# Kernel tuning notes

Hardware: AMD Instinct MI355X
Metric: run time of the kernel (lower is better)

Reference implementation:

```python
import jax, jax.numpy as jnp
import numpy as np

M = 16384      # total flat points per role (8 scenes x 2048 pts)
D = 256        # d_model
H = 4          # heads
K = 16         # knn neighbors
DFF = 1024     # 4*D
LN_EPS = 1e-5


def _ln(x, g, b):
    m = jnp.mean(x, axis=-1, keepdims=True)
    v = jnp.mean((x - m) ** 2, axis=-1, keepdims=True)
    return (x - m) / jnp.sqrt(v + LN_EPS) * g + b


def _knn_block(x, coord, ctx, ctx_coord, idx,
               Wq, Wk, Wv, Wo, g1, b1, pe_w, pe_b,
               W1, bf1, W2, bf2, g2, b2):
    # x: [M,D] query feats; ctx: [N,D] context feats; idx: [M,K] neighbor ids (-1 = invalid)
    m, d = x.shape
    k = idx.shape[1]
    dh = d // H
    valid = idx >= 0
    idx_c = jnp.where(valid, idx, 0)

    xn = _ln(x, g1, b1)
    q = (xn @ Wq).reshape(m, H, dh)                      # [M,H,dh]
    k_all = ctx @ Wk                                     # [N,D]
    v_all = ctx @ Wv                                     # [N,D]

    rel = coord[:, None, :] - ctx_coord[idx_c]           # [M,K,3]
    pe = rel @ pe_w + pe_b                               # [M,K,D] relative position encoding
    kg = (k_all[idx_c] + pe).reshape(m, k, H, dh)        # gathered keys  [M,K,H,dh]
    vg = (v_all[idx_c] + pe).reshape(m, k, H, dh)        # gathered values

    scale = jnp.asarray(1.0 / np.sqrt(dh), x.dtype)
    scores = jnp.einsum('mhd,mkhd->mhk', q, kg) * scale
    scores = jnp.where(valid[:, None, :], scores, jnp.asarray(-1e9, x.dtype))
    attn = jax.nn.softmax(scores, axis=-1)
    out = jnp.einsum('mhk,mkhd->mhd', attn, vg).reshape(m, d) @ Wo
    x = x + out
    h = jax.nn.gelu(_ln(x, g2, b2) @ W1 + bf1)
    return x + (h @ W2 + bf2)


def setup_inputs() -> dict:
    key = jax.random.key(0)
    ks = jax.random.split(key, 24)
    s = 0.02
    nblk = 2  # [0]=self(a), [1]=cross(a,b)
    inp = {
        'feat_a': jax.random.normal(ks[0], (M, D), jnp.float32),
        'coord_a': jax.random.normal(ks[1], (M, 3), jnp.float32),
        'feat_b': jax.random.normal(ks[2], (M, D), jnp.float32),
        'coord_b': jax.random.normal(ks[3], (M, 3), jnp.float32),
        'Wq': jax.random.normal(ks[4], (nblk, D, D), jnp.float32) * s,
        'Wk': jax.random.normal(ks[5], (nblk, D, D), jnp.float32) * s,
        'Wv': jax.random.normal(ks[6], (nblk, D, D), jnp.float32) * s,
        'Wo': jax.random.normal(ks[7], (nblk, D, D), jnp.float32) * s,
        'ln1_g': jnp.ones((nblk, D), jnp.float32),
        'ln1_b': jnp.zeros((nblk, D), jnp.float32),
        'pe_w': jax.random.normal(ks[8], (nblk, 3, D), jnp.float32) * s,
        'pe_b': jnp.zeros((nblk, D), jnp.float32),
        'ffn_w1': jax.random.normal(ks[9], (nblk, D, DFF), jnp.float32) * s,
        'ffn_b1': jnp.zeros((nblk, DFF), jnp.float32),
        'ffn_w2': jax.random.normal(ks[10], (nblk, DFF, D), jnp.float32) * s,
        'ffn_b2': jnp.zeros((nblk, D), jnp.float32),
        'ln2_g': jnp.ones((nblk, D), jnp.float32),
        'ln2_b': jnp.zeros((nblk, D), jnp.float32),
        'knn_a2a': jax.random.randint(ks[11], (M, K), 0, M, jnp.int64 if jax.config.jax_enable_x64 else jnp.int32),
        'knn_a2b': jax.random.randint(ks[12], (M, K), 0, M, jnp.int64 if jax.config.jax_enable_x64 else jnp.int32),
    }
    return inp


def reference(feat_a, coord_a, feat_b, coord_b,
              Wq, Wk, Wv, Wo, ln1_g, ln1_b, pe_w, pe_b,
              ffn_w1, ffn_b1, ffn_w2, ffn_b2, ln2_g, ln2_b,
              knn_a2a, knn_a2b):
    def params(i):
        return (Wq[i], Wk[i], Wv[i], Wo[i], ln1_g[i], ln1_b[i], pe_w[i], pe_b[i],
                ffn_w1[i], ffn_b1[i], ffn_w2[i], ffn_b2[i], ln2_g[i], ln2_b[i])
    # layer 'self(a)': feat[a] = block(feat[a], coord[a], knn_indexes['a2a'])
    fa = _knn_block(feat_a, coord_a, feat_a, coord_a, knn_a2a, *params(0))
    # layer 'cross(a,b)': feat[a] = block(query=feat[a], context=feat[b], knn_indexes['a2b'])
    fa = _knn_block(fa, coord_a, feat_b, coord_b, knn_a2b, *params(1))
    return fa
```

## Files before the change

### kernel.cpp

```cpp
#include <hip/hip_runtime.h>
#include <hip/hip_bf16.h>
#include <stdint.h>

#define MM 16384
#define DD 256
#define HH 4
#define KK 16
#define DFF_ 1024

typedef __attribute__((ext_vector_type(8))) short bf16x8;
typedef __attribute__((ext_vector_type(16))) float f32x16;

__device__ __forceinline__ unsigned short f2bf(float f) {
    unsigned u = __builtin_bit_cast(unsigned, f);
    unsigned r = u + 0x7fffu + ((u >> 16) & 1u);
    return (unsigned short)(r >> 16);
}
__device__ __forceinline__ float bf2f(unsigned short h) {
    unsigned u = ((unsigned)h) << 16;
    return __builtin_bit_cast(float, u);
}
__device__ __forceinline__ float bflo(unsigned u) { return __builtin_bit_cast(float, u << 16); }
__device__ __forceinline__ float bfhi(unsigned u) { return __builtin_bit_cast(float, u & 0xffff0000u); }


__global__ __launch_bounds__(256) void prep_weights(
        const float* __restrict__ Wq, const float* __restrict__ Wk,
        const float* __restrict__ Wv, const float* __restrict__ Wo,
        const float* __restrict__ W1, const float* __restrict__ W2,
        unsigned short* __restrict__ wf) {
    int t = blockIdx.x * blockDim.x + threadIdx.x;
    const float* src; unsigned short* dst;
    int kd, nsrc, rem, blk, e, sect;
    if (t < 131072) { sect = 0; rem = t; blk = rem >> 16; e = rem & 65535;
        src = Wq; dst = wf + blk * 65536; kd = 256; nsrc = 256; }
    else if (t < 262144) { sect = 1; rem = t - 131072; blk = rem >> 16; e = rem & 65535;
        src = Wk; dst = wf + 131072 + blk * 131072; kd = 256; nsrc = 256; }
    else if (t < 393216) { sect = 2; rem = t - 262144; blk = rem >> 16; e = rem & 65535;
        src = Wv; dst = wf + 131072 + blk * 131072; kd = 256; nsrc = 256; }
    else if (t < 524288) { sect = 0; rem = t - 393216; blk = rem >> 16; e = rem & 65535;
        src = Wo; dst = wf + 393216 + blk * 65536; kd = 256; nsrc = 256; }
    else if (t < 1048576) { sect = 0; rem = t - 524288; blk = rem >> 18; e = rem & 262143;
        src = W1; dst = wf + 524288 + blk * 262144; kd = 256; nsrc = 1024; }
    else if (t < 1572864) { sect = 0; rem = t - 1048576; blk = rem >> 18; e = rem & 262143;
        src = W2; dst = wf + 1048576 + blk * 262144; kd = 1024; nsrc = 256; }
    else return;
    int k = e / nsrc;
    int n = e - k * nsrc;
    if (sect == 1) n = (n >> 2) * 8 + (n & 3);
    else if (sect == 2) n = (n >> 2) * 8 + 4 + (n & 3);
    float v = src[(size_t)blk * kd * nsrc + e];
    int off = ((n >> 5) * (kd >> 4) + (k >> 4)) * 512 + (((k >> 3) & 1) * 32 + (n & 31)) * 8 + (k & 7);
    dst[off] = f2bf(v);
}

__global__ __launch_bounds__(256) void ln_to_frag(
        const float* __restrict__ x, const float* __restrict__ g,
        const float* __restrict__ b, unsigned short* __restrict__ out,
        int apply_ln) {
    int wave = threadIdx.x >> 6, lane = threadIdx.x & 63;
    int m = blockIdx.x * 4 + wave;
    const float4 xv = reinterpret_cast<const float4*>(x + (size_t)m * DD)[lane];
    float vals[4] = {xv.x, xv.y, xv.z, xv.w};
    int k0 = lane * 4;
    if (apply_ln) {
        float s = vals[0] + vals[1] + vals[2] + vals[3];
        float sq = vals[0]*vals[0] + vals[1]*vals[1] + vals[2]*vals[2] + vals[3]*vals[3];
        for (int o = 32; o; o >>= 1) { s += __shfl_xor(s, o, 64); sq += __shfl_xor(sq, o, 64); }
        float mean = s * (1.0f / DD);
        float var = sq * (1.0f / DD) - mean * mean;
        float rs = rsqrtf(var + 1e-5f);
        #pragma unroll
        for (int c = 0; c < 4; ++c)
            vals[c] = (vals[c] - mean) * rs * g[k0 + c] + b[k0 + c];
    }
    int chunk = ((m >> 5) * (DD >> 4) + (k0 >> 4)) * 64 + ((k0 >> 3) & 1) * 32 + (m & 31);
    ushort4 o4 = make_ushort4(f2bf(vals[0]), f2bf(vals[1]), f2bf(vals[2]), f2bf(vals[3]));
    *reinterpret_cast<ushort4*>(out + (size_t)chunk * 8 + (k0 & 7)) = o4;
}

constexpr int GOUT_F32 = 0;
constexpr int GOUT_BF16 = 1;
constexpr int GOUT_GELU_FRAG = 2;

template <int KGH>
__device__ __forceinline__ void compute_tile(
        const bf16x8* __restrict__ a0, const bf16x8* __restrict__ a1,
        const bf16x8* __restrict__ b0, const bf16x8* __restrict__ b1,
        f32x16 acc[2][2]) {
    #pragma unroll 4
    for (int g = 0; g < KGH; ++g) {
        bf16x8 av0 = a0[g * 64];
        bf16x8 av1 = a1[g * 64];
        bf16x8 bv0 = b0[g * 64];
        bf16x8 bv1 = b1[g * 64];
        acc[0][0] = __builtin_amdgcn_mfma_f32_32x32x16_bf16(av0, bv0, acc[0][0], 0, 0, 0);
        acc[0][1] = __builtin_amdgcn_mfma_f32_32x32x16_bf16(av0, bv1, acc[0][1], 0, 0, 0);
        acc[1][0] = __builtin_amdgcn_mfma_f32_32x32x16_bf16(av1, bv0, acc[1][0], 0, 0, 0);
        acc[1][1] = __builtin_amdgcn_mfma_f32_32x32x16_bf16(av1, bv1, acc[1][1], 0, 0, 0);
    }
}

template <int KD, int NOUT, int SPLITK, int MODE, bool RESID, bool BIAS>
__global__ __launch_bounds__(SPLITK * 128) void gemm_frag(
        const bf16x8* __restrict__ A, const bf16x8* __restrict__ B,
        void* __restrict__ outp, const float* __restrict__ resid,
        const float* __restrict__ bias, int out_kd) {
    static_assert(MODE != GOUT_GELU_FRAG || SPLITK == 1, "gelu path is 2-wave only");
    constexpr int KG = KD / 16;
    constexpr int KGH = KG / SPLITK;
    __shared__ float lds[SPLITK == 2 ? 2 * 64 * 64 : 2 * 32 * 33];
    int wave = threadIdx.x >> 6, lane = threadIdx.x & 63;
    int mhalf = wave & 1;
    int khalf = (SPLITK == 2) ? (wave >> 1) : 0;
    int m0 = blockIdx.x * 128 + mhalf * 64;
    int n0 = blockIdx.y * 64;
    const bf16x8* a0 = A + ((size_t)(m0 >> 5) * KG + khalf * KGH) * 64 + lane;
    const bf16x8* a1 = a0 + (size_t)KG * 64;
    const bf16x8* b0 = B + ((size_t)(n0 >> 5) * KG + khalf * KGH) * 64 + lane;
    const bf16x8* b1 = b0 + (size_t)KG * 64;
    f32x16 acc[2][2] = {};
    compute_tile<KGH>(a0, a1, b0, b1, acc);
    int col = lane & 31, rq = (lane >> 5) * 4;
    if constexpr (SPLITK == 2) {
        if (khalf == 1) {
            #pragma unroll
            for (int i = 0; i < 2; ++i)
            #pragma unroll
            for (int j = 0; j < 2; ++j)
            #pragma unroll
            for (int r = 0; r < 16; ++r) {
                int row = (r & 3) + 8 * (r >> 2) + rq + i * 32;
                lds[mhalf * 4096 + row * 64 + j * 32 + col] = acc[i][j][r];
            }
        }
        __syncthreads();
        if (khalf == 1) return;
        #pragma unroll
        for (int i = 0; i < 2; ++i)
        #pragma unroll
        for (int j = 0; j < 2; ++j)
        #pragma unroll
        for (int r = 0; r < 16; ++r) {
            int row = (r & 3) + 8 * (r >> 2) + rq + i * 32;
            acc[i][j][r] += lds[mhalf * 4096 + row * 64 + j * 32 + col];
        }
    }
    if constexpr (MODE != GOUT_GELU_FRAG) {
        #pragma unroll
        for (int i = 0; i < 2; ++i)
        #pragma unroll
        for (int j = 0; j < 2; ++j) {
            #pragma unroll
            for (int r = 0; r < 16; ++r) {
                int row = (r & 3) + 8 * (r >> 2) + rq;
                int m = m0 + i * 32 + row;
                int n = n0 + j * 32 + col;
                float v = acc[i][j][r];
                if (BIAS) v += bias[n];
                if (RESID) v += resid[(size_t)m * NOUT + n];
                if (MODE == GOUT_F32) ((float*)outp)[(size_t)m * NOUT + n] = v;
                else ((unsigned short*)outp)[(size_t)m * NOUT + n] = f2bf(v);
            }
        }
    } else {
        float* wlds = &lds[wave * 1056];
        for (int i = 0; i < 2; ++i)
        for (int j = 0; j < 2; ++j) {
            #pragma unroll
            for (int r = 0; r < 16; ++r) {
                int row = (r & 3) + 8 * (r >> 2) + rq;
                int n = n0 + j * 32 + col;
                float v = acc[i][j][r] + bias[n];
                float arg = v * (1.5957691216f + 0.0713548163f * v * v);
                v = v * __frcp_rn(1.0f + __expf(-arg));
                wlds[row * 33 + col] = v;
            }
            #pragma unroll
            for (int it = 0; it < 2; ++it) {
                int task = lane + it * 64;
                int row = task >> 2, cc = task & 3;
                int m = m0 + i * 32 + row;
                int k = n0 + j * 32 + cc * 8;
                float* p = &wlds[row * 33 + cc * 8];
                unsigned short us[8];
                #pragma unroll
                for (int e = 0; e < 8; ++e) us[e] = f2bf(p[e]);
                int chunk = ((m >> 5) * (out_kd >> 4) + (k >> 4)) * 64 + ((k >> 3) & 1) * 32 + (m & 31);
                reinterpret_cast<uint4*>(outp)[chunk] = *reinterpret_cast<uint4*>(us);
            }
        }
    }
}

__global__ __launch_bounds__(256) void gemm_qkv(
        const bf16x8* __restrict__ Aq, const bf16x8* __restrict__ Akv,
        const bf16x8* __restrict__ Bq, const bf16x8* __restrict__ Bkv,
        unsigned short* __restrict__ qout, unsigned short* __restrict__ kvout) {
    constexpr int KG = 16, KGH = 8;
    __shared__ float lds[2 * 64 * 64];
    int wave = threadIdx.x >> 6, lane = threadIdx.x & 63;
    int mhalf = wave & 1, khalf = wave >> 1;
    int y = blockIdx.y;
    bool isQ = y < 4;
    const bf16x8* A = isQ ? Aq : Akv;
    const bf16x8* B = isQ ? Bq : Bkv;
    unsigned short* out = isQ ? qout : kvout;
    int nstride = isQ ? 256 : 512;
    int n0 = (isQ ? y : y - 4) * 64;
    int m0 = blockIdx.x * 128 + mhalf * 64;
    const bf16x8* a0 = A + ((size_t)(m0 >> 5) * KG + khalf * KGH) * 64 + lane;
    const bf16x8* a1 = a0 + (size_t)KG * 64;
    const bf16x8* b0 = B + ((size_t)(n0 >> 5) * KG + khalf * KGH) * 64 + lane;
    const bf16x8* b1 = b0 + (size_t)KG * 64;
    f32x16 acc[2][2] = {};
    compute_tile<KGH>(a0, a1, b0, b1, acc);
    int col = lane & 31, rq = (lane >> 5) * 4;
    if (khalf == 1) {
        #pragma unroll
        for (int i = 0; i < 2; ++i)
        #pragma unroll
        for (int j = 0; j < 2; ++j)
        #pragma unroll
        for (int r = 0; r < 16; ++r) {
            int row = (r & 3) + 8 * (r >> 2) + rq + i * 32;
            lds[mhalf * 4096 + row * 64 + j * 32 + col] = acc[i][j][r];
        }
    }
    __syncthreads();
    if (khalf == 1) return;
    #pragma unroll
    for (int i = 0; i < 2; ++i)
    #pragma unroll
    for (int j = 0; j < 2; ++j)
    #pragma unroll
    for (int r = 0; r < 16; ++r) {
        int row = (r & 3) + 8 * (r >> 2) + rq;
        float v = acc[i][j][r] + lds[mhalf * 4096 + (row + i * 32) * 64 + j * 32 + col];
        out[(size_t)(m0 + i * 32 + row) * nstride + n0 + j * 32 + col] = f2bf(v);
    }
}

__global__ __launch_bounds__(256) void attn_kernel(
        const unsigned short* __restrict__ q, const unsigned short* __restrict__ kv,
        const float* __restrict__ coord, const float* __restrict__ ctx_coord,
        const int* __restrict__ knn,
        const float* __restrict__ pe_w, const float* __restrict__ pe_b,
        unsigned short* __restrict__ out_frag) {
    int wave = threadIdx.x >> 6, lane = threadIdx.x & 63;
    int m = blockIdx.x * 4 + wave;
    int s = lane & 15;
    int d0 = (lane >> 4) * 64 + s * 4;

    ushort4 qv4 = *reinterpret_cast<const ushort4*>(q + (size_t)m * DD + d0);
    float qx = bf2f(qv4.x), qy = bf2f(qv4.y), qz = bf2f(qv4.z), qw = bf2f(qv4.w);
    float4 pw0 = *reinterpret_cast<const float4*>(pe_w + d0);
    float4 pw1 = *reinterpret_cast<const float4*>(pe_w + DD + d0);
    float4 pw2 = *reinterpret_cast<const float4*>(pe_w + 2 * DD + d0);
    float4 pbv = *reinterpret_cast<const float4*>(pe_b + d0);

    float cx = coord[m * 3], cy = coord[m * 3 + 1], cz = coord[m * 3 + 2];
    int myidx = knn[(size_t)m * KK + s];
    int icm = myidx < 0 ? 0 : myidx;
    float rx = cx - ctx_coord[icm * 3];
    float ry = cy - ctx_coord[icm * 3 + 1];
    float rz = cz - ctx_coord[icm * 3 + 2];

    float t0 = qx * pw0.x + qy * pw0.y + qz * pw0.z + qw * pw0.w;
    float t1 = qx * pw1.x + qy * pw1.y + qz * pw1.z + qw * pw1.w;
    float t2 = qx * pw2.x + qy * pw2.y + qz * pw2.z + qw * pw2.w;
    float t3 = qx * pbv.x + qy * pbv.y + qz * pbv.z + qw * pbv.w;
    #pragma unroll
    for (int o = 1; o < 16; o <<= 1) {
        t0 += __shfl_xor(t0, o, 64);
        t1 += __shfl_xor(t1, o, 64);
        t2 += __shfl_xor(t2, o, 64);
        t3 += __shfl_xor(t3, o, 64);
    }

    float sc_own = 0.0f;
    unsigned vlo[KK], vhi[KK];
    #pragma unroll
    for (int j = 0; j < KK; ++j) {
        int ij = __shfl(myidx, j, 64);
        int ic = ij < 0 ? 0 : ij;
        uint4 kvv = *reinterpret_cast<const uint4*>(kv + (size_t)ic * 512 + (size_t)(d0 >> 2) * 8);
        vlo[j] = kvv.z; vhi[j] = kvv.w;
        float p = qx * bflo(kvv.x) + qy * bfhi(kvv.x)
                + qz * bflo(kvv.y) + qw * bfhi(kvv.y);
        p += __shfl_xor(p, 1, 64);
        p += __shfl_xor(p, 2, 64);
        p += __shfl_xor(p, 4, 64);
        p += __shfl_xor(p, 8, 64);
        sc_own = (j == s) ? p : sc_own;
    }
    float corr = rx * t0 + ry * t1 + rz * t2 + t3;
    sc_own = (myidx >= 0) ? (sc_own + corr) * 0.125f : -1e9f;

    float mx = sc_own;
    mx = fmaxf(mx, __shfl_xor(mx, 1, 64));
    mx = fmaxf(mx, __shfl_xor(mx, 2, 64));
    mx = fmaxf(mx, __shfl_xor(mx, 4, 64));
    mx = fmaxf(mx, __shfl_xor(mx, 8, 64));
    float e = __expf(sc_own - mx);
    float sum = e;
    sum += __shfl_xor(sum, 1, 64);
    sum += __shfl_xor(sum, 2, 64);
    sum += __shfl_xor(sum, 4, 64);
    sum += __shfl_xor(sum, 8, 64);
    float w_own = e * __frcp_rn(sum);

    float wrx = w_own * rx, wry = w_own * ry, wrz = w_own * rz;
    #pragma unroll
    for (int o = 1; o < 16; o <<= 1) {
        wrx += __shfl_xor(wrx, o, 64);
        wry += __shfl_xor(wry, o, 64);
        wrz += __shfl_xor(wrz, o, 64);
    }

    int gbase = lane & 48;
    float ax = 0.f, ay = 0.f, az = 0.f, aw = 0.f;
    #pragma unroll
    for (int j = 0; j < KK; ++j) {
        float wj = __shfl(w_own, gbase + j, 64);
        ax += wj * bflo(vlo[j]);
        ay += wj * bfhi(vlo[j]);
        az += wj * bflo(vhi[j]);
        aw += wj * bfhi(vhi[j]);
    }
    ax += wrx * pw0.x + wry * pw1.x + wrz * pw2.x + pbv.x;
    ay += wrx * pw0.y + wry * pw1.y + wrz * pw2.y + pbv.y;
    az += wrx * pw0.z + wry * pw1.z + wrz * pw2.z + pbv.z;
    aw += wrx * pw0.w + wry * pw1.w + wrz * pw2.w + pbv.w;

    ushort4 o4 = make_ushort4(f2bf(ax), f2bf(ay), f2bf(az), f2bf(aw));
    int chunk = ((m >> 5) * (DD >> 4) + (d0 >> 4)) * 64 + ((d0 >> 3) & 1) * 32 + (m & 31);
    *reinterpret_cast<ushort4*>(out_frag + (size_t)chunk * 8 + (d0 & 7)) = o4;
}

extern "C" void kernel_launch(void* const* d_in, const int* in_sizes, int n_in,
                              void* d_out, int out_size, void* d_ws, size_t ws_size,
                              hipStream_t stream) {
    const float* feat_a = (const float*)d_in[0];
    const float* coord_a = (const float*)d_in[1];
    const float* feat_b = (const float*)d_in[2];
    const float* coord_b = (const float*)d_in[3];
    const float* Wq = (const float*)d_in[4];
    const float* Wk = (const float*)d_in[5];
    const float* Wv = (const float*)d_in[6];
    const float* Wo = (const float*)d_in[7];
    const float* ln1_g = (const float*)d_in[8];
    const float* ln1_b = (const float*)d_in[9];
    const float* pe_w = (const float*)d_in[10];
    const float* pe_b = (const float*)d_in[11];
    const float* W1 = (const float*)d_in[12];
    const float* b1 = (const float*)d_in[13];
    const float* W2 = (const float*)d_in[14];
    const float* b2 = (const float*)d_in[15];
    const float* ln2_g = (const float*)d_in[16];
    const float* ln2_b = (const float*)d_in[17];
    const int* knn_a2a = (const int*)d_in[18];
    const int* knn_a2b = (const int*)d_in[19];

    char* ws = (char*)d_ws;
    unsigned short* wfrag = (unsigned short*)ws;
    float* xmid = (float*)(ws + (4ull << 20));
    float* xout0 = (float*)(ws + (20ull << 20));
    unsigned short* qbuf = (unsigned short*)(ws + (36ull << 20));
    unsigned short* kvbuf = (unsigned short*)(ws + (52ull << 20));
    unsigned short* xnf = (unsigned short*)(ws + (68ull << 20));
    unsigned short* ctxf = (unsigned short*)(ws + (76ull << 20));
    unsigned short* attnf = (unsigned short*)(ws + (84ull << 20));
    unsigned short* geluf = (unsigned short*)(ws + (36ull << 20));

    const unsigned short* WQF = wfrag;
    const unsigned short* KVF = wfrag + 131072;
    const unsigned short* WOF = wfrag + 393216;
    const unsigned short* W1F = wfrag + 524288;
    const unsigned short* W2F = wfrag + 1048576;

    prep_weights<<<(1572864 + 255) / 256, 256, 0, stream>>>(Wq, Wk, Wv, Wo, W1, W2, wfrag);

    for (int blk = 0; blk < 2; ++blk) {
        const float* x_in = blk ? xout0 : feat_a;
        const float* ctx = blk ? feat_b : feat_a;
        const float* ccrd = blk ? coord_b : coord_a;
        const int* knn = blk ? knn_a2b : knn_a2a;
        float* x_out_final = blk ? (float*)d_out : xout0;

        ln_to_frag<<<MM / 4, 256, 0, stream>>>(ctx, nullptr, nullptr, ctxf, 0);
        ln_to_frag<<<MM / 4, 256, 0, stream>>>(x_in, ln1_g + blk * DD, ln1_b + blk * DD, xnf, 1);

        gemm_qkv<<<dim3(MM / 128, 12), 256, 0, stream>>>(
            (const bf16x8*)xnf, (const bf16x8*)ctxf,
            (const bf16x8*)(WQF + blk * 65536), (const bf16x8*)(KVF + blk * 131072),
            qbuf, kvbuf);

        attn_kernel<<<MM / 4, 256, 0, stream>>>(qbuf, kvbuf, coord_a, ccrd, knn,
                                                pe_w + blk * 3 * DD, pe_b + blk * DD, attnf);

        gemm_frag<256, 256, 2, GOUT_F32, true, false><<<dim3(MM / 128, 4), 256, 0, stream>>>(
            (const bf16x8*)attnf, (const bf16x8*)(WOF + blk * 65536), xmid, x_in, nullptr, 0);

        ln_to_frag<<<MM / 4, 256, 0, stream>>>(xmid, ln2_g + blk * DD, ln2_b + blk * DD, xnf, 1);

        gemm_frag<256, 1024, 1, GOUT_GELU_FRAG, false, true><<<dim3(MM / 128, 16), 128, 0, stream>>>(
            (const bf16x8*)xnf, (const bf16x8*)(W1F + blk * 262144), geluf, nullptr,
            b1 + blk * DFF_, 1024);

        gemm_frag<1024, 256, 2, GOUT_F32, true, true><<<dim3(MM / 128, 4), 256, 0, stream>>>(
            (const bf16x8*)geluf, (const bf16x8*)(W2F + blk * 262144), x_out_final, xmid,
            b2 + blk * DD, 0);
    }
}
```

Before: 365.9 us.

## Fuse LayerNorm into residual GEMM epilogues with full-row tiles

Replaces the output-projection and FFN2 GEMMs with a 512-thread kernel where each block computes a full 64x256 row tile. Row statistics are reduced across waves through shared memory, so the next LayerNorm (ln2, or the next block's ln1) is applied in the epilogue and written directly in fragment layout. This removes separate ln_to_frag launches and their re-read of the fp32 activations. In exchange it uses more shared memory, adds extra barriers, and launches fewer, larger blocks, which may lower occupancy.

```diff
diff --git a/kernel.cpp b/kernel.cpp
--- a/kernel.cpp
+++ b/kernel.cpp
@@ -79,10 +79,6 @@
     *reinterpret_cast<ushort4*>(out + (size_t)chunk * 8 + (k0 & 7)) = o4;
 }
 
-constexpr int GOUT_F32 = 0;
-constexpr int GOUT_BF16 = 1;
-constexpr int GOUT_GELU_FRAG = 2;
-
 template <int KGH>
 __device__ __forceinline__ void compute_tile(
         const bf16x8* __restrict__ a0, const bf16x8* __restrict__ a1,
@@ -101,80 +97,100 @@
     }
 }
 
-template <int KD, int NOUT, int SPLITK, int MODE, bool RESID, bool BIAS>
-__global__ __launch_bounds__(SPLITK * 128) void gemm_frag(
+template <int KD, bool BIAS, bool DO_LN>
+__global__ __launch_bounds__(512) void gemm_ln(
         const bf16x8* __restrict__ A, const bf16x8* __restrict__ B,
-        void* __restrict__ outp, const float* __restrict__ resid,
-        const float* __restrict__ bias, int out_kd) {
-    static_assert(MODE != GOUT_GELU_FRAG || SPLITK == 1, "gelu path is 2-wave only");
-    constexpr int KG = KD / 16;
-    constexpr int KGH = KG / SPLITK;
-    __shared__ float lds[SPLITK == 2 ? 2 * 64 * 64 : 2 * 32 * 33];
+        const float* __restrict__ resid, const float* __restrict__ bias,
+        const float* __restrict__ lng, const float* __restrict__ lnb,
+        float* __restrict__ out_f32, unsigned short* __restrict__ out_frag) {
+    constexpr int KG = KD / 16, KGH = KG / 2;
+    __shared__ float lds[4 * 64 * 64 + 512 + 128];
+    float* lnsum = lds + 16384;
+    float* lnsq  = lnsum + 256;
+    float* lnstat = lnsq + 256;
     int wave = threadIdx.x >> 6, lane = threadIdx.x & 63;
-    int mhalf = wave & 1;
-    int khalf = (SPLITK == 2) ? (wave >> 1) : 0;
-    int m0 = blockIdx.x * 128 + mhalf * 64;
-    int n0 = blockIdx.y * 64;
-    const bf16x8* a0 = A + ((size_t)(m0 >> 5) * KG + khalf * KGH) * 64 + lane;
+    int wn = wave & 3, kh = wave >> 2;
+    int m0 = blockIdx.x * 64;
+    int n0 = wn * 64;
+    const bf16x8* a0 = A + ((size_t)(m0 >> 5) * KG + kh * KGH) * 64 + lane;
     const bf16x8* a1 = a0 + (size_t)KG * 64;
-    const bf16x8* b0 = B + ((size_t)(n0 >> 5) * KG + khalf * KGH) * 64 + lane;
+    const bf16x8* b0 = B + ((size_t)(n0 >> 5) * KG + kh * KGH) * 64 + lane;
     const bf16x8* b1 = b0 + (size_t)KG * 64;
     f32x16 acc[2][2] = {};
     compute_tile<KGH>(a0, a1, b0, b1, acc);
     int col = lane & 31, rq = (lane >> 5) * 4;
-    if constexpr (SPLITK == 2) {
-        if (khalf == 1) {
+    float* skbuf = &lds[wn * 4096];
+    if (kh == 1) {
+        #pragma unroll
+        for (int i = 0; i < 2; ++i)
+        #pragma unroll
+        for (int j = 0; j < 2; ++j)
+        #pragma unroll
+        for (int r = 0; r < 16; ++r) {
+            int rl = (r & 3) + 8 * (r >> 2) + rq;
+            skbuf[(i * 32 + rl) * 64 + j * 32 + col] = acc[i][j][r];
+        }
+    }
+    __syncthreads();
+    if (kh == 0) {
+        #pragma unroll
+        for (int i = 0; i < 2; ++i)
+        #pragma unroll
+        for (int j = 0; j < 2; ++j)
+        #pragma unroll
+        for (int r = 0; r < 16; ++r) {
+            int rl = (r & 3) + 8 * (r >> 2) + rq;
+            int m = m0 + i * 32 + rl;
+            int n = n0 + j * 32 + col;
+            float v = acc[i][j][r] + skbuf[(i * 32 + rl) * 64 + j * 32 + col];
+            if (BIAS) v += bias[n];
+            v += resid[(size_t)m * 256 + n];
+            out_f32[(size_t)m * 256 + n] = v;
+            acc[i][j][r] = v;
+        }
+    }
+    if constexpr (DO_LN) {
+        if (kh == 0) {
             #pragma unroll
             for (int i = 0; i < 2; ++i)
             #pragma unroll
-            for (int j = 0; j < 2; ++j)
-            #pragma unroll
             for (int r = 0; r < 16; ++r) {
-                int row = (r & 3) + 8 * (r >> 2) + rq + i * 32;
-                lds[mhalf * 4096 + row * 64 + j * 32 + col] = acc[i][j][r];
+                float v0 = acc[i][0][r], v1 = acc[i][1][r];
+                float p = v0 + v1, q = v0 * v0 + v1 * v1;
+                #pragma unroll
+                for (int o = 1; o < 32; o <<= 1) {
+                    p += __shfl_xor(p, o, 64);
+                    q += __shfl_xor(q, o, 64);
+                }
+                if (col == 0) {
+                    int row64 = i * 32 + (r & 3) + 8 * (r >> 2) + rq;
+                    lnsum[wn * 64 + row64] = p;
+                    lnsq[wn * 64 + row64] = q;
+                }
             }
         }
         __syncthreads();
-        if (khalf == 1) return;
-        #pragma unroll
-        for (int i = 0; i < 2; ++i)
-        #pragma unroll
-        for (int j = 0; j < 2; ++j)
-        #pragma unroll
-        for (int r = 0; r < 16; ++r) {
-            int row = (r & 3) + 8 * (r >> 2) + rq + i * 32;
-            acc[i][j][r] += lds[mhalf * 4096 + row * 64 + j * 32 + col];
-        }
-    }
-    if constexpr (MODE != GOUT_GELU_FRAG) {
-        #pragma unroll
-        for (int i = 0; i < 2; ++i)
-        #pragma unroll
-        for (int j = 0; j < 2; ++j) {
-            #pragma unroll
-            for (int r = 0; r < 16; ++r) {
-                int row = (r & 3) + 8 * (r >> 2) + rq;
-                int m = m0 + i * 32 + row;
-                int n = n0 + j * 32 + col;
-                float v = acc[i][j][r];
-                if (BIAS) v += bias[n];
-                if (RESID) v += resid[(size_t)m * NOUT + n];
-                if (MODE == GOUT_F32) ((float*)outp)[(size_t)m * NOUT + n] = v;
-                else ((unsigned short*)outp)[(size_t)m * NOUT + n] = f2bf(v);
-            }
-        }
-    } else {
-        float* wlds = &lds[wave * 1056];
+        if (wave == 0) {
+            int row = lane;
+            float s = lnsum[row] + lnsum[64 + row] + lnsum[128 + row] + lnsum[192 + row];
+            float q = lnsq[row] + lnsq[64 + row] + lnsq[128 + row] + lnsq[192 + row];
+            float mean = s * (1.0f / 256.0f);
+            float var = q * (1.0f / 256.0f) - mean * mean;
+            lnstat[row * 2] = mean;
+            lnstat[row * 2 + 1] = rsqrtf(var + 1e-5f);
+        }
+        __syncthreads();
+        if (kh == 1) return;
         for (int i = 0; i < 2; ++i)
         for (int j = 0; j < 2; ++j) {
             #pragma unroll
             for (int r = 0; r < 16; ++r) {
-                int row = (r & 3) + 8 * (r >> 2) + rq;
+                int rl = (r & 3) + 8 * (r >> 2) + rq;
+                int row64 = i * 32 + rl;
+                float mean = lnstat[row64 * 2], rs = lnstat[row64 * 2 + 1];
                 int n = n0 + j * 32 + col;
-                float v = acc[i][j][r] + bias[n];
-                float arg = v * (1.5957691216f + 0.0713548163f * v * v);
-                v = v * __frcp_rn(1.0f + __expf(-arg));
-                wlds[row * 33 + col] = v;
+                float vln = (acc[i][j][r] - mean) * rs * lng[n] + lnb[n];
+                skbuf[rl * 33 + col] = vln;
             }
             #pragma unroll
             for (int it = 0; it < 2; ++it) {
@@ -182,13 +198,56 @@
                 int row = task >> 2, cc = task & 3;
                 int m = m0 + i * 32 + row;
                 int k = n0 + j * 32 + cc * 8;
-                float* p = &wlds[row * 33 + cc * 8];
+                float* p = &skbuf[row * 33 + cc * 8];
                 unsigned short us[8];
                 #pragma unroll
                 for (int e = 0; e < 8; ++e) us[e] = f2bf(p[e]);
-                int chunk = ((m >> 5) * (out_kd >> 4) + (k >> 4)) * 64 + ((k >> 3) & 1) * 32 + (m & 31);
-                reinterpret_cast<uint4*>(outp)[chunk] = *reinterpret_cast<uint4*>(us);
+                int chunk = ((m >> 5) * 16 + (k >> 4)) * 64 + ((k >> 3) & 1) * 32 + (m & 31);
+                reinterpret_cast<uint4*>(out_frag)[chunk] = *reinterpret_cast<uint4*>(us);
             }
+        }
+    }
+}
+
+__global__ __launch_bounds__(128) void gemm_gelu(
+        const bf16x8* __restrict__ A, const bf16x8* __restrict__ B,
+        unsigned short* __restrict__ outp, const float* __restrict__ bias) {
+    constexpr int KG = 16;
+    __shared__ float lds[2 * 32 * 33];
+    int wave = threadIdx.x >> 6, lane = threadIdx.x & 63;
+    int m0 = blockIdx.x * 128 + wave * 64;
+    int n0 = blockIdx.y * 64;
+    const bf16x8* a0 = A + ((size_t)(m0 >> 5) * KG) * 64 + lane;
+    const bf16x8* a1 = a0 + (size_t)KG * 64;
+    const bf16x8* b0 = B + ((size_t)(n0 >> 5) * KG) * 64 + lane;
+    const bf16x8* b1 = b0 + (size_t)KG * 64;
+    f32x16 acc[2][2] = {};
+    compute_tile<KG>(a0, a1, b0, b1, acc);
+    int col = lane & 31, rq = (lane >> 5) * 4;
+    float* wlds = &lds[wave * 1056];
+    for (int i = 0; i < 2; ++i)
+    for (int j = 0; j < 2; ++j) {
+        #pragma unroll
+        for (int r = 0; r < 16; ++r) {
+            int row = (r & 3) + 8 * (r >> 2) + rq;
+            int n = n0 + j * 32 + col;
+            float v = acc[i][j][r] + bias[n];
+            float arg = v * (1.5957691216f + 0.0713548163f * v * v);
+            v = v * __frcp_rn(1.0f + __expf(-arg));
+            wlds[row * 33 + col] = v;
+        }
+        #pragma unroll
+        for (int it = 0; it < 2; ++it) {
+            int task = lane + it * 64;
+            int row = task >> 2, cc = task & 3;
+            int m = m0 + i * 32 + row;
+            int k = n0 + j * 32 + cc * 8;
+            float* p = &wlds[row * 33 + cc * 8];
+            unsigned short us[8];
+            #pragma unroll
+            for (int e = 0; e < 8; ++e) us[e] = f2bf(p[e]);
+            int chunk = ((m >> 5) * 64 + (k >> 4)) * 64 + ((k >> 3) & 1) * 32 + (m & 31);
+            reinterpret_cast<uint4*>(outp)[chunk] = *reinterpret_cast<uint4*>(us);
         }
     }
 }
@@ -381,35 +440,36 @@
 
     prep_weights<<<(1572864 + 255) / 256, 256, 0, stream>>>(Wq, Wk, Wv, Wo, W1, W2, wfrag);
 
-    for (int blk = 0; blk < 2; ++blk) {
-        const float* x_in = blk ? xout0 : feat_a;
-        const float* ctx = blk ? feat_b : feat_a;
-        const float* ccrd = blk ? coord_b : coord_a;
-        const int* knn = blk ? knn_a2b : knn_a2a;
-        float* x_out_final = blk ? (float*)d_out : xout0;
-
-        ln_to_frag<<<MM / 4, 256, 0, stream>>>(ctx, nullptr, nullptr, ctxf, 0);
-        ln_to_frag<<<MM / 4, 256, 0, stream>>>(x_in, ln1_g + blk * DD, ln1_b + blk * DD, xnf, 1);
-
-        gemm_qkv<<<dim3(MM / 128, 12), 256, 0, stream>>>(
-            (const bf16x8*)xnf, (const bf16x8*)ctxf,
-            (const bf16x8*)(WQF + blk * 65536), (const bf16x8*)(KVF + blk * 131072),
-            qbuf, kvbuf);
-
-        attn_kernel<<<MM / 4, 256, 0, stream>>>(qbuf, kvbuf, coord_a, ccrd, knn,
-                                                pe_w + blk * 3 * DD, pe_b + blk * DD, attnf);
-
-        gemm_frag<256, 256, 2, GOUT_F32, true, false><<<dim3(MM / 128, 4), 256, 0, stream>>>(
-            (const bf16x8*)attnf, (const bf16x8*)(WOF + blk * 65536), xmid, x_in, nullptr, 0);
-
-        ln_to_frag<<<MM / 4, 256, 0, stream>>>(xmid, ln2_g + blk * DD, ln2_b + blk * DD, xnf, 1);
-
-        gemm_frag<256, 1024, 1, GOUT_GELU_FRAG, false, true><<<dim3(MM / 128, 16), 128, 0, stream>>>(
-            (const bf16x8*)xnf, (const bf16x8*)(W1F + blk * 262144), geluf, nullptr,
-            b1 + blk * DFF_, 1024);
-
-        gemm_frag<1024, 256, 2, GOUT_F32, true, true><<<dim3(MM / 128, 4), 256, 0, stream>>>(
-            (const bf16x8*)geluf, (const bf16x8*)(W2F + blk * 262144), x_out_final, xmid,
-            b2 + blk * DD, 0);
-    }
-}
+    ln_to_frag<<<MM / 4, 256, 0, stream>>>(feat_a, nullptr, nullptr, ctxf, 0);
+    ln_to_frag<<<MM / 4, 256, 0, stream>>>(feat_a, ln1_g, ln1_b, xnf, 1);
+
+    gemm_qkv<<<dim3(MM / 128, 12), 256, 0, stream>>>(
+        (const bf16x8*)xnf, (const bf16x8*)ctxf,
+        (const bf16x8*)WQF, (const bf16x8*)KVF, qbuf, kvbuf);
+    attn_kernel<<<MM / 4, 256, 0, stream>>>(qbuf, kvbuf, coord_a, coord_a, knn_a2a,
+                                            pe_w, pe_b, attnf);
+    gemm_ln<256, false, true><<<MM / 64, 512, 0, stream>>>(
+        (const bf16x8*)attnf, (const bf16x8*)WOF, feat_a, nullptr,
+        ln2_g, ln2_b, xmid, xnf);
+    gemm_gelu<<<dim3(MM / 128, 16), 128, 0, stream>>>(
+        (const bf16x8*)xnf, (const bf16x8*)W1F, geluf, b1);
+    gemm_ln<1024, true, true><<<MM / 64, 512, 0, stream>>>(
+        (const bf16x8*)geluf, (const bf16x8*)(W2F), xmid, b2,
+        ln1_g + DD, ln1_b + DD, xout0, xnf);
+
+    ln_to_frag<<<MM / 4, 256, 0, stream>>>(feat_b, nullptr, nullptr, ctxf, 0);
+
+    gemm_qkv<<<dim3(MM / 128, 12), 256, 0, stream>>>(
+        (const bf16x8*)xnf, (const bf16x8*)ctxf,
+        (const bf16x8*)(WQF + 65536), (const bf16x8*)(KVF + 131072), qbuf, kvbuf);
+    attn_kernel<<<MM / 4, 256, 0, stream>>>(qbuf, kvbuf, coord_a, coord_b, knn_a2b,
+                                            pe_w + 3 * DD, pe_b + DD, attnf);
+    gemm_ln<256, false, true><<<MM / 64, 512, 0, stream>>>(
+        (const bf16x8*)attnf, (const bf16x8*)(WOF + 65536), xout0, nullptr,
+        ln2_g + DD, ln2_b + DD, xmid, xnf);
+    gemm_gelu<<<dim3(MM / 128, 16), 128, 0, stream>>>(
+        (const bf16x8*)xnf, (const bf16x8*)(W1F + 262144), geluf, b1 + DFF_);
+    gemm_ln<1024, true, false><<<MM / 64, 512, 0, stream>>>(
+        (const bf16x8*)geluf, (const bf16x8*)(W2F + 262144), xmid, b2 + DD,
+        nullptr, nullptr, (float*)d_out, nullptr);
+}
```

Result: slower. 383.7 us (+4.9%).
